# Performance work log

Measured on AMD Instinct MI355X. Metric: run time of the kernel, lower is better.

## Reference

```python
import jax, jax.numpy as jnp
import numpy as np

VOCAB, EMBED, HIDDEN = 32000, 100, 128
B, T = 1024, 256


def setup_inputs() -> dict:
    key = jax.random.key(0)
    ks = jax.random.split(key, 8)
    s_e = 1.0 / np.sqrt(HIDDEN)  # torch nn.RNN init scale
    x = jax.random.randint(ks[0], (B, T), 0, VOCAB, dtype=jnp.int64)
    emb = jax.random.normal(ks[1], (VOCAB, EMBED), dtype=jnp.float32)
    W_ih = jax.random.uniform(ks[2], (HIDDEN, EMBED), jnp.float32, -s_e, s_e)
    W_hh = jax.random.uniform(ks[3], (HIDDEN, HIDDEN), jnp.float32, -s_e, s_e)
    b_ih = jax.random.uniform(ks[4], (HIDDEN,), jnp.float32, -s_e, s_e)
    b_hh = jax.random.uniform(ks[5], (HIDDEN,), jnp.float32, -s_e, s_e)
    s_f = 1.0 / np.sqrt(HIDDEN)
    W_fc = jax.random.uniform(ks[6], (VOCAB, HIDDEN), jnp.float32, -s_f, s_f)
    b_fc = jax.random.uniform(ks[7], (VOCAB,), jnp.float32, -s_f, s_f)
    return {"x": x, "emb": emb, "W_ih": W_ih, "W_hh": W_hh,
            "b_ih": b_ih, "b_hh": b_hh, "W_fc": W_fc, "b_fc": b_fc}


def reference(x, emb, W_ih, W_hh, b_ih, b_hh, W_fc, b_fc):
    # embedding lookup: [B,T] -> [B,T,E]
    embedded = emb[x]
    # precompute input projections for all timesteps: [B,T,H]
    xp = jnp.einsum('bte,he->bth', embedded, W_ih) + b_ih + b_hh
    xp_t = jnp.swapaxes(xp, 0, 1)  # [T,B,H]

    def step(h, xt):
        h = jnp.tanh(xt + h @ W_hh.T)
        return h, None

    h0 = jnp.zeros((x.shape[0], W_hh.shape[0]), dtype=emb.dtype)
    h_last, _ = jax.lax.scan(step, h0, xp_t)
    # final-step linear head: [B,H] -> [B,V]
    return h_last @ W_fc.T + b_fc
```

## Files before the change

kernel.cpp:

```cpp
#include <hip/hip_runtime.h>
#include <hip/hip_bf16.h>

#define V_ 32000
#define E_ 100
#define H_ 128
#define B_ 1024
#define T_ 256

typedef float f32x4 __attribute__((ext_vector_type(4)));
typedef int   i32x4 __attribute__((ext_vector_type(4)));
typedef __bf16 bf16x8 __attribute__((ext_vector_type(8)));
typedef __bf16 bf16x4 __attribute__((ext_vector_type(4)));

__device__ __forceinline__ f32x4 mfma16(bf16x8 a, bf16x8 b, f32x4 c) {
    return __builtin_amdgcn_mfma_f32_16x16x32_bf16(a, b, c, 0, 0, 0);
}

__global__ __launch_bounds__(512, 1) void k0_pp(
    const float* __restrict__ emb, const float* __restrict__ Wih,
    const float* __restrict__ bih, const float* __restrict__ bhh,
    __bf16* __restrict__ pp)
{
    const int tid = threadIdx.x;
    const int lane = tid & 63, w = tid >> 6;
    const int nt = w >> 1;
    const int mh = w & 1;
    const int v0 = blockIdx.x * 64;
    const int sub = lane >> 4, rc = lane & 15;
    const f32x4 z = {0.f, 0.f, 0.f, 0.f};

    bf16x8 af[4][4];
#pragma unroll
    for (int m = 0; m < 4; ++m)
#pragma unroll
        for (int kc = 0; kc < 4; ++kc) {
            int row = (mh * 4 + m) * 16 + rc;
            int k0 = kc * 32 + sub * 8;
            const float* s = Wih + (size_t)row * E_ + k0;
            f32x4 p0 = (k0 + 4 <= E_) ? *(const f32x4*)s : z;
            f32x4 p1 = (k0 + 8 <= E_) ? *(const f32x4*)(s + 4) : z;
            bf16x8 h8;
#pragma unroll
            for (int e = 0; e < 4; ++e) {
                h8[e] = (__bf16)p0[e];
                h8[4 + e] = (__bf16)p1[e];
            }
            af[m][kc] = h8;
        }

    bf16x8 bf[4];
#pragma unroll
    for (int kc = 0; kc < 4; ++kc) {
        int vrow = v0 + nt * 16 + rc;
        int k0 = kc * 32 + sub * 8;
        const float* s = emb + (size_t)vrow * E_ + k0;
        f32x4 p0 = (k0 + 4 <= E_) ? *(const f32x4*)s : z;
        f32x4 p1 = (k0 + 8 <= E_) ? *(const f32x4*)(s + 4) : z;
        bf16x8 h8;
#pragma unroll
        for (int e = 0; e < 4; ++e) {
            h8[e] = (__bf16)p0[e];
            h8[4 + e] = (__bf16)p1[e];
        }
        bf[kc] = h8;
    }

    f32x4 acc[4];
#pragma unroll
    for (int m = 0; m < 4; ++m) {
        int h0 = (mh * 4 + m) * 16 + sub * 4;
        acc[m] = *(const f32x4*)&bih[h0] + *(const f32x4*)&bhh[h0];
    }
#pragma unroll
    for (int kc = 0; kc < 4; ++kc)
#pragma unroll
        for (int m = 0; m < 4; ++m)
            acc[m] = mfma16(af[m][kc], bf[kc], acc[m]);

#pragma unroll
    for (int m = 0; m < 4; ++m) {
        int v = v0 + nt * 16 + rc;
        int h0 = (mh * 4 + m) * 16 + sub * 4;
        bf16x4 o;
#pragma unroll
        for (int r = 0; r < 4; ++r) o[r] = (__bf16)acc[m][r];
        *(bf16x4*)&pp[(size_t)v * H_ + h0] = o;
    }
}

__global__ __launch_bounds__(512, 1) void k2_rnn(
    const int* __restrict__ x, const __bf16* __restrict__ pp,
    const float* __restrict__ Whh, __bf16* __restrict__ hg)
{
    __shared__ __align__(16) __bf16 Hg[2][2048];
    const int tid = threadIdx.x;
    const int lane = tid & 63, w = tid >> 6;
    const int bi = blockIdx.x;
    const int b0 = bi * 16;
    const int sub = lane >> 4, c = lane & 15;

    bf16x8 wah[4];
#pragma unroll
    for (int kc = 0; kc < 4; ++kc) {
        const float* src = Whh + (size_t)(w * 16 + c) * H_ + kc * 32 + sub * 8;
        f32x4 p0 = *(const f32x4*)src, p1 = *(const f32x4*)(src + 4);
        bf16x8 h8;
#pragma unroll
        for (int e = 0; e < 4; ++e) {
            h8[e] = (__bf16)p0[e];
            h8[4 + e] = (__bf16)p1[e];
        }
        wah[kc] = h8;
    }

    if (tid < 256) {
        bf16x8 z8;
#pragma unroll
        for (int e = 0; e < 8; ++e) z8[e] = (__bf16)0.0f;
        *(bf16x8*)&Hg[0][tid * 8] = z8;
    }
    __syncthreads();

    const int i0 = w * 16 + sub * 4;
    const int* xrow = x + (size_t)(b0 + c) * T_;
    const __bf16* ppi = pp + i0;

    const int wb = (((w >> 1) * 64 + ((w & 1) * 2 + (sub >> 1)) * 16 + c) << 3)
                 + (sub & 1) * 4;

    bf16x4 h4;

#define K2_STEP(PK, XREG, GBODY) do {                                       \
        const __bf16* Hp = &Hg[PK][0];                                      \
        bf16x8 hb0 = *(const bf16x8*)(Hp + lane * 8);                       \
        bf16x8 hb1 = *(const bf16x8*)(Hp + 512 + lane * 8);                 \
        bf16x8 hb2 = *(const bf16x8*)(Hp + 1024 + lane * 8);                \
        bf16x8 hb3 = *(const bf16x8*)(Hp + 1536 + lane * 8);                \
        f32x4 xf;                                                           \
        _Pragma("unroll")                                                   \
        for (int r = 0; r < 4; ++r) xf[r] = (float)XREG[r];                 \
        f32x4 zz = {0.f, 0.f, 0.f, 0.f};                                    \
        f32x4 a0 = mfma16(wah[0], hb0, xf);                                 \
        f32x4 a1 = mfma16(wah[1], hb1, zz);                                 \
        a0 = mfma16(wah[2], hb2, a0);                                       \
        a1 = mfma16(wah[3], hb3, a1);                                       \
        GBODY;                                                              \
        f32x4 s = a0 + a1;                                                  \
        _Pragma("unroll")                                                   \
        for (int r = 0; r < 4; ++r) {                                       \
            float e;                                                        \
            asm("v_exp_f32 %0, %1" : "=v"(e) : "v"(s[r] * 2.8853900817779268f)); \
            float ep1 = e + 1.0f;                                           \
            float rcp;                                                      \
            asm("v_rcp_f32 %0, %1" : "=v"(rcp) : "v"(ep1));                 \
            h4[r] = (__bf16)(1.0f - 2.0f * rcp);                            \
        }                                                                   \
        *(bf16x4*)&Hg[(PK) ^ 1][wb] = h4;                                   \
        asm volatile("s_waitcnt lgkmcnt(0)" ::: "memory");                  \
        __builtin_amdgcn_s_barrier();                                       \
        __builtin_amdgcn_sched_barrier(0);                                  \
    } while (0)

    i32x4 xs0 = *(const i32x4*)(xrow);
    bf16x4 xc0 = *(const bf16x4*)(ppi + (size_t)xs0[0] * H_);
    bf16x4 xc1 = *(const bf16x4*)(ppi + (size_t)xs0[1] * H_);
    bf16x4 xc2 = *(const bf16x4*)(ppi + (size_t)xs0[2] * H_);
    bf16x4 xc3 = *(const bf16x4*)(ppi + (size_t)xs0[3] * H_);
    i32x4 xsA = *(const i32x4*)(xrow + 4);

    for (int j = 0; j < T_ / 4; ++j) {
        bf16x4 xn0, xn1, xn2, xn3;
        i32x4 xsB;
        int tg = 4 * (j + 2);
        const int* xnext = xrow + (tg <= T_ - 4 ? tg : T_ - 4);

        K2_STEP(0, xc0, { xn0 = *(const bf16x4*)(ppi + (size_t)xsA[0] * H_); });
        K2_STEP(1, xc1, { xn1 = *(const bf16x4*)(ppi + (size_t)xsA[1] * H_); });
        K2_STEP(0, xc2, { xn2 = *(const bf16x4*)(ppi + (size_t)xsA[2] * H_); });
        K2_STEP(1, xc3, { xn3 = *(const bf16x4*)(ppi + (size_t)xsA[3] * H_);
                          xsB = *(const i32x4*)(xnext); });

        xc0 = xn0; xc1 = xn1; xc2 = xn2; xc3 = xn3;
        xsA = xsB;
    }
#undef K2_STEP

    *(bf16x4*)&hg[(size_t)(bi >> 3) * 16384 + (size_t)(bi & 7) * 2048 + wb] = h4;
}

__global__ __launch_bounds__(512, 1) void k3_head(
    const float* __restrict__ Wfc, const __bf16* __restrict__ hg,
    const float* __restrict__ bfc, float* __restrict__ out)
{
    const int tid = threadIdx.x;
    const int lane = tid & 63, w = tid >> 6;
    const int gv = blockIdx.x;
    const int v0 = gv * 128;
    const int sub = lane >> 4, rc = lane & 15;
    const int mt0 = (w & 3) * 2, nt0 = (w >> 2) * 4;

    bf16x8 af[2][4];
#pragma unroll
    for (int m = 0; m < 2; ++m)
#pragma unroll
        for (int kc = 0; kc < 4; ++kc) {
            int row = v0 + (mt0 + m) * 16 + rc;
            const float* src = Wfc + (size_t)row * H_ + (kc * 4 + sub) * 8;
            f32x4 p0 = *(const f32x4*)src, p1 = *(const f32x4*)(src + 4);
            bf16x8 h8;
#pragma unroll
            for (int e = 0; e < 4; ++e) {
                h8[e] = (__bf16)p0[e];
                h8[4 + e] = (__bf16)p1[e];
            }
            af[m][kc] = h8;
        }

    f32x4 bias4[2];
#pragma unroll
    for (int m = 0; m < 2; ++m)
        bias4[m] = *(const f32x4*)&bfc[v0 + (mt0 + m) * 16 + sub * 4];

    for (int bt = 0; bt < 8; ++bt) {
        const int b0 = bt * 128;
        f32x4 acc[2][4];
#pragma unroll
        for (int m = 0; m < 2; ++m)
#pragma unroll
            for (int n = 0; n < 4; ++n) acc[m][n] = (f32x4){0.f, 0.f, 0.f, 0.f};

#pragma unroll
        for (int kc = 0; kc < 4; ++kc) {
            bf16x8 bf[4];
#pragma unroll
            for (int n = 0; n < 4; ++n)
                bf[n] = *(const bf16x8*)&hg[(size_t)bt * 16384
                          + (size_t)(((nt0 + n) * 256) + kc * 64 + lane) * 8];
#pragma unroll
            for (int n = 0; n < 4; ++n)
#pragma unroll
                for (int m = 0; m < 2; ++m)
                    acc[m][n] = mfma16(af[m][kc], bf[n], acc[m][n]);
        }
#pragma unroll
        for (int n = 0; n < 4; ++n)
#pragma unroll
            for (int m = 0; m < 2; ++m) {
                f32x4 v = acc[m][n] + bias4[m];
                float* dst = out + (size_t)(b0 + (nt0 + n) * 16 + rc) * V_
                                 + v0 + (mt0 + m) * 16 + sub * 4;
                *(f32x4*)dst = v;
            }
    }
}

extern "C" void kernel_launch(void* const* d_in, const int* in_sizes, int n_in,
                              void* d_out, int out_size, void* d_ws, size_t ws_size,
                              hipStream_t stream) {
    const int*   x   = (const int*)d_in[0];
    const float* emb = (const float*)d_in[1];
    const float* Wih = (const float*)d_in[2];
    const float* Whh = (const float*)d_in[3];
    const float* bih = (const float*)d_in[4];
    const float* bhh = (const float*)d_in[5];
    const float* Wfc = (const float*)d_in[6];
    const float* bfc = (const float*)d_in[7];
    float* out = (float*)d_out;

    const size_t SZ_HG = 262144;
    const size_t SZ_PP = (size_t)V_ * H_ * 2;

    char* wsb = (char*)d_ws;
    size_t off = 0;
    auto take = [&](size_t n) -> char* {
        char* p = wsb + off;
        off += (n + 255) & ~(size_t)255;
        return p;
    };
    auto fits = [&](size_t n) { return off + n + 256 <= ws_size; };

    __bf16* hgp = (__bf16*)take(SZ_HG);
    __bf16* pp = fits(SZ_PP) ? (__bf16*)take(SZ_PP) : (__bf16*)d_out;

    k0_pp<<<dim3(500), 512, 0, stream>>>(emb, Wih, bih, bhh, pp);
    k2_rnn<<<dim3(64), 512, 0, stream>>>(x, pp, Whh, hgp);
    k3_head<<<dim3(250), 512, 0, stream>>>(Wfc, hgp, bfc, out);
}
```

Baseline: 146.0 us.

## Stage gathered input projections into LDS via async global_load_lds ring buffer

The per-timestep gather of precomputed input projections moves from each lane loading its own bf16x4 from global memory into registers to four waves issuing direct global-to-LDS DMA loads into a 4-slot ring buffer. Lanes then read their slice from LDS, and vmcnt waits are folded into the existing per-step barrier. The aim is to cut the number of scattered global load instructions on the serial recurrence path and take register staging of future steps off that path. In exchange it adds LDS traffic and more complex vmcnt accounting, which could break correctness or stall if the counts are off.

```diff
diff --git a/kernel.cpp b/kernel.cpp
--- a/kernel.cpp
+++ b/kernel.cpp
@@ -93,6 +93,7 @@
     const float* __restrict__ Whh, __bf16* __restrict__ hg)
 {
     __shared__ __align__(16) __bf16 Hg[2][2048];
+    __shared__ __align__(16) __bf16 Hx[4][2048];
     const int tid = threadIdx.x;
     const int lane = tid & 63, w = tid >> 6;
     const int bi = blockIdx.x;
@@ -119,32 +120,38 @@
         for (int e = 0; e < 8; ++e) z8[e] = (__bf16)0.0f;
         *(bf16x8*)&Hg[0][tid * 8] = z8;
     }
-    __syncthreads();
 
     const int i0 = w * 16 + sub * 4;
     const int* xrow = x + (size_t)(b0 + c) * T_;
-    const __bf16* ppi = pp + i0;
+    const int sk = w * 32 + ((lane >> 4) & 3) * 8;
 
     const int wb = (((w >> 1) * 64 + ((w & 1) * 2 + (sub >> 1)) * 16 + c) << 3)
                  + (sub & 1) * 4;
 
     bf16x4 h4;
 
-#define K2_STEP(PK, XREG, GBODY) do {                                       \
+#define DMA(XV, SLOT)                                                        \
+    do { if (w < 4) {                                                        \
+        const __bf16* gsrc = pp + (size_t)(XV) * H_ + sk;                    \
+        __builtin_amdgcn_global_load_lds(gsrc, &Hx[SLOT][w * 512], 16, 0, 0);\
+    } } while (0)
+
+#define K2_STEP(PK, SK, VMS, STAGE) do {                                    \
         const __bf16* Hp = &Hg[PK][0];                                      \
         bf16x8 hb0 = *(const bf16x8*)(Hp + lane * 8);                       \
         bf16x8 hb1 = *(const bf16x8*)(Hp + 512 + lane * 8);                 \
         bf16x8 hb2 = *(const bf16x8*)(Hp + 1024 + lane * 8);                \
         bf16x8 hb3 = *(const bf16x8*)(Hp + 1536 + lane * 8);                \
+        bf16x4 xtv = *(const bf16x4*)&Hx[SK][wb];                           \
+        STAGE;                                                              \
         f32x4 xf;                                                           \
         _Pragma("unroll")                                                   \
-        for (int r = 0; r < 4; ++r) xf[r] = (float)XREG[r];                 \
+        for (int r = 0; r < 4; ++r) xf[r] = (float)xtv[r];                  \
         f32x4 zz = {0.f, 0.f, 0.f, 0.f};                                    \
         f32x4 a0 = mfma16(wah[0], hb0, xf);                                 \
         f32x4 a1 = mfma16(wah[1], hb1, zz);                                 \
         a0 = mfma16(wah[2], hb2, a0);                                       \
         a1 = mfma16(wah[3], hb3, a1);                                       \
-        GBODY;                                                              \
         f32x4 s = a0 + a1;                                                  \
         _Pragma("unroll")                                                   \
         for (int r = 0; r < 4; ++r) {                                       \
@@ -156,34 +163,33 @@
             h4[r] = (__bf16)(1.0f - 2.0f * rcp);                            \
         }                                                                   \
         *(bf16x4*)&Hg[(PK) ^ 1][wb] = h4;                                   \
-        asm volatile("s_waitcnt lgkmcnt(0)" ::: "memory");                  \
+        asm volatile("s_waitcnt vmcnt(" VMS ") lgkmcnt(0)" ::: "memory");   \
         __builtin_amdgcn_s_barrier();                                       \
         __builtin_amdgcn_sched_barrier(0);                                  \
     } while (0)
 
-    i32x4 xs0 = *(const i32x4*)(xrow);
-    bf16x4 xc0 = *(const bf16x4*)(ppi + (size_t)xs0[0] * H_);
-    bf16x4 xc1 = *(const bf16x4*)(ppi + (size_t)xs0[1] * H_);
-    bf16x4 xc2 = *(const bf16x4*)(ppi + (size_t)xs0[2] * H_);
-    bf16x4 xc3 = *(const bf16x4*)(ppi + (size_t)xs0[3] * H_);
-    i32x4 xsA = *(const i32x4*)(xrow + 4);
+    i32x4 xs0, xs1;
+    if (w < 4) {
+        xs0 = *(const i32x4*)(xrow);
+        DMA(xs0[0], 0);
+        DMA(xs0[1], 1);
+        DMA(xs0[2], 2);
+        xs1 = *(const i32x4*)(xrow + 4);
+    }
+    __syncthreads();
 
     for (int j = 0; j < T_ / 4; ++j) {
-        bf16x4 xn0, xn1, xn2, xn3;
-        i32x4 xsB;
-        int tg = 4 * (j + 2);
-        const int* xnext = xrow + (tg <= T_ - 4 ? tg : T_ - 4);
-
-        K2_STEP(0, xc0, { xn0 = *(const bf16x4*)(ppi + (size_t)xsA[0] * H_); });
-        K2_STEP(1, xc1, { xn1 = *(const bf16x4*)(ppi + (size_t)xsA[1] * H_); });
-        K2_STEP(0, xc2, { xn2 = *(const bf16x4*)(ppi + (size_t)xsA[2] * H_); });
-        K2_STEP(1, xc3, { xn3 = *(const bf16x4*)(ppi + (size_t)xsA[3] * H_);
-                          xsB = *(const i32x4*)(xnext); });
-
-        xc0 = xn0; xc1 = xn1; xc2 = xn2; xc3 = xn3;
-        xsA = xsB;
+        const int* xnext = xrow + ((4 * (j + 2) <= T_ - 4) ? 4 * (j + 2) : (T_ - 4));
+        i32x4 xs2;
+        K2_STEP(0, 0, "2", { DMA(xs0[3], 3); });
+        K2_STEP(1, 1, "2", { DMA(xs1[0], 0); });
+        K2_STEP(0, 2, "2", { DMA(xs1[1], 1); });
+        K2_STEP(1, 3, "3", { DMA(xs1[2], 2);
+                             if (w < 4) xs2 = *(const i32x4*)(xnext); });
+        if (w < 4) { xs0 = xs1; xs1 = xs2; }
     }
 #undef K2_STEP
+#undef DMA
 
     *(bf16x4*)&hg[(size_t)(bi >> 3) * 16384 + (size_t)(bi & 7) * 2048 + wb] = h4;
 }
```

Result: slower. 156.3 us (+7.1%).
